# Kernel tuning notes

Measured on AMD Instinct MI355X. Metric: run time of the kernel, lower is better.

Reference implementation:

```python
import jax, jax.numpy as jnp
import numpy as np
import math

FILT_LEN = 10  # all Farras / dual filters are 10-tap
INV_SQRT2 = 1.0 / math.sqrt(2.0)

# Farras first-stage analysis filters (fs_farras), shape [tree(2), lo/hi(2), 10]
_F = 0.08838834764832
_G = 0.01122679215254
_H = 0.69587998903400
FAF_NP = np.array([
    [[0.0, -_F, _F, _H, _H, _F, -_F, _G, _G, 0.0],
     [0.0, -_G, _G, _F, _F, -_H, _H, -_F, -_F, 0.0]],
    [[_G, _G, -_F, _F, _H, _H, _F, -_F, 0.0, 0.0],
     [0.0, 0.0, -_F, -_F, _H, -_H, _F, _F, _G, -_G]]], dtype=np.float32)
# Kingsbury Q-shift dual filters (duelfilt / dualfilt1), shape [tree(2), lo/hi(2), 10]
_A = 0.03516384
_B = 0.08832942
_C = 0.23389032
_D = 0.76027237
_E = 0.58751830
_K = 0.11430184
AF_NP = np.array([
    [[_A, 0.0, -_B, _C, _D, _E, 0.0, -_K, 0.0, 0.0],
     [0.0, 0.0, -_K, 0.0, _E, -_D, _C, _B, 0.0, -_A]],
    [[0.0, 0.0, -_K, 0.0, _E, _D, _C, -_B, 0.0, _A],
     [-_A, 0.0, _B, _C, -_D, _E, 0.0, -_K, 0.0, 0.0]]], dtype=np.float32)


def _afb_axis(x, lo_f, hi_f, axis):
    """1D circular analysis filter bank along spatial `axis` (1=rows, 2=cols).
    x: (B,H,W,C). Returns (lo, hi), each halved along `axis`.
    Math: x <- cshift(x,-L); y = downsample2(fullconv(x,f)); wrap-add first L taps.
    """
    N = x.shape[axis]
    L = FILT_LEN // 2
    C = x.shape[-1]
    x = jnp.roll(x, -L, axis=axis)

    def conv(f):
        kf = f[::-1].astype(x.dtype)  # lax does correlation -> flip for convolution
        if axis == 1:
            ker = jnp.tile(kf.reshape(FILT_LEN, 1, 1, 1), (1, 1, 1, C))
            pad = [(FILT_LEN - 1, FILT_LEN - 1), (0, 0)]
            strides = (2, 1)
        else:
            ker = jnp.tile(kf.reshape(1, FILT_LEN, 1, 1), (1, 1, 1, C))
            pad = [(0, 0), (FILT_LEN - 1, FILT_LEN - 1)]
            strides = (1, 2)
        return jax.lax.conv_general_dilated(
            x, ker, window_strides=strides, padding=pad,
            dimension_numbers=('NHWC', 'HWIO', 'NHWC'),
            feature_group_count=C)  # depthwise, per-channel identical filter

    def wrap(y):
        # y has N//2 + L samples along axis; fold periodic tail into head
        head = (jax.lax.slice_in_dim(y, 0, L, axis=axis)
                + jax.lax.slice_in_dim(y, N // 2, N // 2 + L, axis=axis))
        body = jax.lax.slice_in_dim(y, L, N // 2, axis=axis)
        return jnp.concatenate([head, body], axis=axis)

    return wrap(conv(lo_f)), wrap(conv(hi_f))


def afb2d(x, lo_row, hi_row, lo_col, hi_col):
    """2D separable analysis filter bank: returns (lo, [lohi, hilo, hihi])."""
    Lr, Hr = _afb_axis(x, lo_row, hi_row, axis=1)
    lo, w0 = _afb_axis(Lr, lo_col, hi_col, axis=2)
    w1, w2 = _afb_axis(Hr, lo_col, hi_col, axis=2)
    return lo, [w0, w1, w2]


def _add_sub(a, b):
    return (a + b) * INV_SQRT2, (a - b) * INV_SQRT2


def _dtcwt(x, Faf, af, level):
    x = x / 2
    w = [[[None, None] for _ in range(2)] for _ in range(level + 1)]
    for m in range(2):
        for n in range(2):
            lo, w[0][m][n] = afb2d(x, Faf[m, 0], Faf[m, 1], Faf[n, 0], Faf[n, 1])
            for j in range(1, level):
                lo, w[j][m][n] = afb2d(lo, af[m, 0], af[m, 1], af[n, 0], af[n, 1])
            w[level][m][n] = lo
    # combine dual trees into (approx) complex pairs
    for j in range(level):
        for s in range(3):
            w[j][0][0][s], w[j][1][1][s] = _add_sub(w[j][0][0][s], w[j][1][1][s])
            w[j][0][1][s], w[j][1][0][s] = _add_sub(w[j][0][1][s], w[j][1][0][s])
    # multiscale 2x2 tiling reassembly (concat=True path)
    wc = w
    for j in range(level - 1, 0, -1):
        for a in range(2):
            for b in range(2):
                wc[j][a][b] = jnp.concatenate([
                    jnp.concatenate([wc[j + 1][a][b], wc[j][a][b][0]], axis=2),
                    jnp.concatenate([wc[j][a][b][1], wc[j][a][b][2]], axis=2)], axis=1)
    tiles = []
    for a in range(2):
        for b in range(2):
            tiles.append(jnp.concatenate([
                jnp.concatenate([wc[1][a][b], wc[0][a][b][0]], axis=2),
                jnp.concatenate([wc[0][a][b][1], wc[0][a][b][2]], axis=2)], axis=1))
    w0, w1, w2, w3 = tiles
    return jnp.concatenate([jnp.concatenate([w0, w1], axis=2),
                            jnp.concatenate([w2, w3], axis=2)], axis=1)


def setup_inputs() -> dict:
    key = jax.random.key(0)
    x = jax.random.normal(key, (8, 512, 512, 3), dtype=jnp.float32)
    return {"x": x, "Faf": jnp.asarray(FAF_NP), "af": jnp.asarray(AF_NP), "level": 3}


def reference(x, Faf, af, level):
    return _dtcwt(x, Faf, af, int(level))
```

## Files before the change

kernel.cpp:

```cpp
#include <hip/hip_runtime.h>


#define FF 0.08838834764832f
#define GG 0.01122679215254f
#define HHc 0.69587998903400f
#define AAc 0.03516384f
#define BBc 0.08832942f
#define CCc 0.23389032f
#define DDc 0.76027237f
#define EEc 0.58751830f
#define KKc 0.11430184f

__device__ __constant__ float c_filt[2][2][2][10] = {
  {
    { {0.f,-FF, FF, HHc, HHc, FF,-FF, GG, GG, 0.f},
      {0.f,-GG, GG, FF, FF,-HHc, HHc,-FF,-FF, 0.f} },
    { {GG, GG,-FF, FF, HHc, HHc, FF,-FF, 0.f, 0.f},
      {0.f, 0.f,-FF,-FF, HHc,-HHc, FF, FF, GG,-GG} }
  },
  {
    { {AAc, 0.f,-BBc, CCc, DDc, EEc, 0.f,-KKc, 0.f, 0.f},
      {0.f, 0.f,-KKc, 0.f, EEc,-DDc, CCc, BBc, 0.f,-AAc} },
    { {0.f, 0.f,-KKc, 0.f, EEc, DDc, CCc,-BBc, 0.f, AAc},
      {-AAc, 0.f, BBc, CCc,-DDc, EEc, 0.f,-KKc, 0.f, 0.f} }
  }
};

__device__ __forceinline__ void cmb(float& a, float& b) {
  const float k = 0.70710678118654752440f;
  const float s = (a + b) * k, d = (a - b) * k;
  a = s; b = d;
}

template<int LVL, int N, int Ho, int Wo>
__global__ __launch_bounds__(256) void fused_level(
    const float* __restrict__ src,
    float* __restrict__ llout,
    float* __restrict__ out)
{
  constexpr int half = N / 2;
  constexpr int W2 = 2 * Wo + 8;
  constexpr int NF = (LVL == 0) ? 4 : 8;
  constexpr size_t ZS = (size_t)8 * N * N * 3;
  constexpr size_t ZOUT = (size_t)8 * half * half * 3;
  __shared__ float inter[Ho][W2][3][NF];

  const int jt = blockIdx.x, it = blockIdx.y, b = blockIdx.z;
  const int i0 = it * Ho, j0 = jt * Wo;
  const int tid = threadIdx.x;

  constexpr int itemsA = Ho * W2 * 3;
  for (int item = tid; item < itemsA; item += 256) {
    const int il = item / (W2 * 3);
    const int rm = item - il * (W2 * 3);
    const int wl = rm / 3;
    const int c  = rm - wl * 3;
    const int colg = (2 * j0 - 4 + wl) & (N - 1);
    const int ig = i0 + il;
    if (LVL == 0) {
      const float* sp = src + (((size_t)b * N) * N + colg) * 3 + c;
      float a0 = 0.f, a1 = 0.f, a2 = 0.f, a3 = 0.f;
#pragma unroll
      for (int t = 0; t < 10; ++t) {
        const int row = (2 * ig + 5 - t) & (N - 1);
        const float v = sp[(size_t)row * (N * 3)];
        a0 += c_filt[0][0][0][t] * v;
        a1 += c_filt[0][0][1][t] * v;
        a2 += c_filt[0][1][0][t] * v;
        a3 += c_filt[0][1][1][t] * v;
      }
      inter[il][wl][c][0] = a0 * 0.5f;
      inter[il][wl][c][1] = a1 * 0.5f;
      inter[il][wl][c][2] = a2 * 0.5f;
      inter[il][wl][c][3] = a3 * 0.5f;
    } else {
      float acc[8];
#pragma unroll
      for (int f = 0; f < 8; ++f) acc[f] = 0.f;
#pragma unroll
      for (int z = 0; z < 4; ++z) {
        const int m = z >> 1;
        const float* sp = src + (size_t)z * ZS + (((size_t)b * N) * N + colg) * 3 + c;
#pragma unroll
        for (int t = 0; t < 10; ++t) {
          const int row = (2 * ig + 5 - t) & (N - 1);
          const float v = sp[(size_t)row * (N * 3)];
          acc[2 * z]     += c_filt[1][m][0][t] * v;
          acc[2 * z + 1] += c_filt[1][m][1][t] * v;
        }
      }
#pragma unroll
      for (int f = 0; f < 8; ++f) inter[il][wl][c][f] = acc[f];
    }
  }
  __syncthreads();

  constexpr int itemsB = Ho * Wo * 3;
  for (int item = tid; item < itemsB; item += 256) {
    const int il = item / (Wo * 3);
    const int rm = item - il * (Wo * 3);
    const int jl = rm / 3;
    const int c  = rm - jl * 3;
    float LL[4] = {}, LH[4] = {}, HL[4] = {}, HH[4] = {};
#pragma unroll
    for (int s = 0; s < 10; ++s) {
      const int wl = 2 * jl + 9 - s;
      if (LVL == 0) {
        const float lo0 = inter[il][wl][c][0], hi0 = inter[il][wl][c][1];
        const float lo1 = inter[il][wl][c][2], hi1 = inter[il][wl][c][3];
#pragma unroll
        for (int n = 0; n < 2; ++n) {
          const float fl = c_filt[0][n][0][s], fh = c_filt[0][n][1][s];
          LL[n]     += fl * lo0; LH[n]     += fh * lo0;
          HL[n]     += fl * hi0; HH[n]     += fh * hi0;
          LL[2 + n] += fl * lo1; LH[2 + n] += fh * lo1;
          HL[2 + n] += fl * hi1; HH[2 + n] += fh * hi1;
        }
      } else {
#pragma unroll
        for (int z = 0; z < 4; ++z) {
          const int n = z & 1;
          const float fl = c_filt[1][n][0][s], fh = c_filt[1][n][1][s];
          const float a = inter[il][wl][c][2 * z], d = inter[il][wl][c][2 * z + 1];
          LL[z] += fl * a; LH[z] += fh * a;
          HL[z] += fl * d; HH[z] += fh * d;
        }
      }
    }
    cmb(LH[0], LH[3]); cmb(LH[1], LH[2]);
    cmb(HL[0], HL[3]); cmb(HL[1], HL[2]);
    cmb(HH[0], HH[3]); cmb(HH[1], HH[2]);
    const int ig = i0 + il, jg = j0 + jl;
    const size_t outB = (size_t)b * (1024u * 1024u * 3u);
#pragma unroll
    for (int z = 0; z < 4; ++z) {
      const int m = z >> 1, n = z & 1;
      const int r0 = m * 512, c0 = n * 512;
      if (LVL == 2)
        out[outB + ((size_t)(r0 + ig) * 1024 + (c0 + jg)) * 3 + c] = LL[z];
      else
        llout[(size_t)z * ZOUT + (((size_t)b * half + ig) * half + jg) * 3 + c] = LL[z];
      out[outB + ((size_t)(r0 + ig) * 1024 + (c0 + half + jg)) * 3 + c] = LH[z];
      out[outB + ((size_t)(r0 + half + ig) * 1024 + (c0 + jg)) * 3 + c] = HL[z];
      out[outB + ((size_t)(r0 + half + ig) * 1024 + (c0 + half + jg)) * 3 + c] = HH[z];
    }
  }
}

extern "C" void kernel_launch(void* const* d_in, const int* in_sizes, int n_in,
                              void* d_out, int out_size, void* d_ws, size_t ws_size,
                              hipStream_t stream) {
  (void)in_sizes; (void)n_in; (void)out_size; (void)ws_size;
  const float* x = (const float*)d_in[0];
  float* out = (float*)d_out;
  float* LL1 = (float*)d_ws;
  float* LL2 = LL1 + 6291456;

  fused_level<0, 512, 8, 32><<<dim3(8, 32, 8), 256, 0, stream>>>(x, LL1, out);
  fused_level<1, 256, 8, 16><<<dim3(8, 16, 8), 256, 0, stream>>>(LL1, LL2, out);
  fused_level<2, 128, 8, 16><<<dim3(4, 8, 8), 256, 0, stream>>>(LL2, nullptr, out);
}
```

Measured before the change: 167.5 us.

## Vectorize row-filter loads with float4 and swizzle shared intermediate layout

The row-filter stage now treats each image row as a flat channel-interleaved float array. Each thread loads four consecutive floats with one float4 access instead of one scalar per (column, channel). The intermediate subbands are stored in shared memory as XOR-swizzled float4 entries, which reduces bank conflicts and allows vector reads. The column stage now gives each thread all three channels of one output pixel. This cuts index arithmetic and shared loads, but leaves half the threads idle at levels 1 and 2 and raises register pressure.

After: 166.2 us. No clear change (-0.8%).

```diff
diff --git a/kernel.cpp b/kernel.cpp
--- a/kernel.cpp
+++ b/kernel.cpp
@@ -32,6 +32,8 @@
   a = s; b = d;
 }
 
+__device__ __forceinline__ int swz4(int f4) { return f4 ^ ((f4 >> 3) & 7); }
+
 template<int LVL, int N, int Ho, int Wo>
 __global__ __launch_bounds__(256) void fused_level(
     const float* __restrict__ src,
@@ -41,108 +43,143 @@
   constexpr int half = N / 2;
   constexpr int W2 = 2 * Wo + 8;
   constexpr int NF = (LVL == 0) ? 4 : 8;
+  constexpr int ROWF = 3 * N;
+  constexpr int FL = 3 * W2;
+  constexpr int SIF4 = (3 * W2 * NF) / 4 + 4;
   constexpr size_t ZS = (size_t)8 * N * N * 3;
   constexpr size_t ZOUT = (size_t)8 * half * half * 3;
-  __shared__ float inter[Ho][W2][3][NF];
+  __shared__ __align__(16) float inter[Ho * SIF4 * 4];
 
   const int jt = blockIdx.x, it = blockIdx.y, b = blockIdx.z;
   const int i0 = it * Ho, j0 = jt * Wo;
   const int tid = threadIdx.x;
 
-  constexpr int itemsA = Ho * W2 * 3;
-  for (int item = tid; item < itemsA; item += 256) {
-    const int il = item / (W2 * 3);
-    const int rm = item - il * (W2 * 3);
-    const int wl = rm / 3;
-    const int c  = rm - wl * 3;
-    const int colg = (2 * j0 - 4 + wl) & (N - 1);
+  int base = (2 * j0 - 4) * 3;
+  if (base < 0) base += ROWF;
+
+  constexpr int I4 = FL / 4;
+  for (int item = tid; item < Ho * I4; item += 256) {
+    const int il = item / I4;
+    const int q4 = (item - il * I4) * 4;
+    int fg = base + q4;
+    if (fg >= ROWF) fg -= ROWF;
     const int ig = i0 + il;
-    if (LVL == 0) {
-      const float* sp = src + (((size_t)b * N) * N + colg) * 3 + c;
-      float a0 = 0.f, a1 = 0.f, a2 = 0.f, a3 = 0.f;
+    float acc[NF][4];
+#pragma unroll
+    for (int f = 0; f < NF; ++f)
+#pragma unroll
+      for (int k = 0; k < 4; ++k) acc[f][k] = 0.f;
+
+    if constexpr (LVL == 0) {
+      const float* sp = src + (size_t)b * N * ROWF + fg;
 #pragma unroll
       for (int t = 0; t < 10; ++t) {
-        const int row = (2 * ig + 5 - t) & (N - 1);
-        const float v = sp[(size_t)row * (N * 3)];
-        a0 += c_filt[0][0][0][t] * v;
-        a1 += c_filt[0][0][1][t] * v;
-        a2 += c_filt[0][1][0][t] * v;
-        a3 += c_filt[0][1][1][t] * v;
+        const int r = (2 * ig + 5 - t) & (N - 1);
+        const float4 v = *(const float4*)(sp + (size_t)r * ROWF);
+#pragma unroll
+        for (int f = 0; f < 4; ++f) {
+          const float fc = c_filt[0][f >> 1][f & 1][t];
+          acc[f][0] += fc * v.x; acc[f][1] += fc * v.y;
+          acc[f][2] += fc * v.z; acc[f][3] += fc * v.w;
+        }
       }
-      inter[il][wl][c][0] = a0 * 0.5f;
-      inter[il][wl][c][1] = a1 * 0.5f;
-      inter[il][wl][c][2] = a2 * 0.5f;
-      inter[il][wl][c][3] = a3 * 0.5f;
+#pragma unroll
+      for (int f = 0; f < 4; ++f)
+#pragma unroll
+        for (int k = 0; k < 4; ++k) acc[f][k] *= 0.5f;
     } else {
-      float acc[8];
-#pragma unroll
-      for (int f = 0; f < 8; ++f) acc[f] = 0.f;
 #pragma unroll
       for (int z = 0; z < 4; ++z) {
         const int m = z >> 1;
-        const float* sp = src + (size_t)z * ZS + (((size_t)b * N) * N + colg) * 3 + c;
+        const float* sp = src + (size_t)z * ZS + (size_t)b * N * ROWF + fg;
 #pragma unroll
         for (int t = 0; t < 10; ++t) {
-          const int row = (2 * ig + 5 - t) & (N - 1);
-          const float v = sp[(size_t)row * (N * 3)];
-          acc[2 * z]     += c_filt[1][m][0][t] * v;
-          acc[2 * z + 1] += c_filt[1][m][1][t] * v;
+          const int r = (2 * ig + 5 - t) & (N - 1);
+          const float4 v = *(const float4*)(sp + (size_t)r * ROWF);
+          const float fl = c_filt[1][m][0][t], fh = c_filt[1][m][1][t];
+          acc[2 * z][0] += fl * v.x; acc[2 * z][1] += fl * v.y;
+          acc[2 * z][2] += fl * v.z; acc[2 * z][3] += fl * v.w;
+          acc[2 * z + 1][0] += fh * v.x; acc[2 * z + 1][1] += fh * v.y;
+          acc[2 * z + 1][2] += fh * v.z; acc[2 * z + 1][3] += fh * v.w;
         }
       }
+    }
 #pragma unroll
-      for (int f = 0; f < 8; ++f) inter[il][wl][c][f] = acc[f];
+    for (int k = 0; k < 4; ++k) {
+      const int fq = q4 + k;
+      if constexpr (NF == 4) {
+        float4 w = make_float4(acc[0][k], acc[1][k], acc[2][k], acc[3][k]);
+        *(float4*)&inter[(il * SIF4 + swz4(fq)) * 4] = w;
+      } else {
+        float4 w0 = make_float4(acc[0][k], acc[1][k], acc[2][k], acc[3][k]);
+        float4 w1 = make_float4(acc[4][k], acc[5][k], acc[6][k], acc[7][k]);
+        *(float4*)&inter[(il * SIF4 + swz4(2 * fq)) * 4] = w0;
+        *(float4*)&inter[(il * SIF4 + swz4(2 * fq + 1)) * 4] = w1;
+      }
     }
   }
   __syncthreads();
 
-  constexpr int itemsB = Ho * Wo * 3;
-  for (int item = tid; item < itemsB; item += 256) {
-    const int il = item / (Wo * 3);
-    const int rm = item - il * (Wo * 3);
-    const int jl = rm / 3;
-    const int c  = rm - jl * 3;
-    float LL[4] = {}, LH[4] = {}, HL[4] = {}, HH[4] = {};
+  if (tid < Ho * Wo) {
+    const int il = tid / Wo, jl = tid - (tid / Wo) * Wo;
+    float LL[4][3] = {}, LH[4][3] = {}, HL[4][3] = {}, HH[4][3] = {};
 #pragma unroll
     for (int s = 0; s < 10; ++s) {
       const int wl = 2 * jl + 9 - s;
-      if (LVL == 0) {
-        const float lo0 = inter[il][wl][c][0], hi0 = inter[il][wl][c][1];
-        const float lo1 = inter[il][wl][c][2], hi1 = inter[il][wl][c][3];
 #pragma unroll
-        for (int n = 0; n < 2; ++n) {
-          const float fl = c_filt[0][n][0][s], fh = c_filt[0][n][1][s];
-          LL[n]     += fl * lo0; LH[n]     += fh * lo0;
-          HL[n]     += fl * hi0; HH[n]     += fh * hi0;
-          LL[2 + n] += fl * lo1; LH[2 + n] += fh * lo1;
-          HL[2 + n] += fl * hi1; HH[2 + n] += fh * hi1;
-        }
-      } else {
+      for (int c = 0; c < 3; ++c) {
+        if constexpr (LVL == 0) {
+          const int f4 = wl * 3 + c;
+          const float4 v = *(const float4*)&inter[(il * SIF4 + swz4(f4)) * 4];
+          const float a0 = v.x, d0 = v.y, a1 = v.z, d1 = v.w;
 #pragma unroll
-        for (int z = 0; z < 4; ++z) {
-          const int n = z & 1;
-          const float fl = c_filt[1][n][0][s], fh = c_filt[1][n][1][s];
-          const float a = inter[il][wl][c][2 * z], d = inter[il][wl][c][2 * z + 1];
-          LL[z] += fl * a; LH[z] += fh * a;
-          HL[z] += fl * d; HH[z] += fh * d;
+          for (int n = 0; n < 2; ++n) {
+            const float fl = c_filt[0][n][0][s], fh = c_filt[0][n][1][s];
+            LL[n][c] += fl * a0; LH[n][c] += fh * a0;
+            HL[n][c] += fl * d0; HH[n][c] += fh * d0;
+            LL[2 + n][c] += fl * a1; LH[2 + n][c] += fh * a1;
+            HL[2 + n][c] += fl * d1; HH[2 + n][c] += fh * d1;
+          }
+        } else {
+          const int f4 = (wl * 3 + c) * 2;
+          const float4 v0 = *(const float4*)&inter[(il * SIF4 + swz4(f4)) * 4];
+          const float4 v1 = *(const float4*)&inter[(il * SIF4 + swz4(f4 + 1)) * 4];
+          const float az[4] = {v0.x, v0.z, v1.x, v1.z};
+          const float dz[4] = {v0.y, v0.w, v1.y, v1.w};
+#pragma unroll
+          for (int z = 0; z < 4; ++z) {
+            const int n = z & 1;
+            const float fl = c_filt[1][n][0][s], fh = c_filt[1][n][1][s];
+            LL[z][c] += fl * az[z]; LH[z][c] += fh * az[z];
+            HL[z][c] += fl * dz[z]; HH[z][c] += fh * dz[z];
+          }
         }
       }
     }
-    cmb(LH[0], LH[3]); cmb(LH[1], LH[2]);
-    cmb(HL[0], HL[3]); cmb(HL[1], HL[2]);
-    cmb(HH[0], HH[3]); cmb(HH[1], HH[2]);
+#pragma unroll
+    for (int c = 0; c < 3; ++c) {
+      cmb(LH[0][c], LH[3][c]); cmb(LH[1][c], LH[2][c]);
+      cmb(HL[0][c], HL[3][c]); cmb(HL[1][c], HL[2][c]);
+      cmb(HH[0][c], HH[3][c]); cmb(HH[1][c], HH[2][c]);
+    }
     const int ig = i0 + il, jg = j0 + jl;
     const size_t outB = (size_t)b * (1024u * 1024u * 3u);
 #pragma unroll
     for (int z = 0; z < 4; ++z) {
       const int m = z >> 1, n = z & 1;
       const int r0 = m * 512, c0 = n * 512;
-      if (LVL == 2)
-        out[outB + ((size_t)(r0 + ig) * 1024 + (c0 + jg)) * 3 + c] = LL[z];
+      float* pLL;
+      if constexpr (LVL == 2)
+        pLL = out + outB + ((size_t)(r0 + ig) * 1024 + (c0 + jg)) * 3;
       else
-        llout[(size_t)z * ZOUT + (((size_t)b * half + ig) * half + jg) * 3 + c] = LL[z];
-      out[outB + ((size_t)(r0 + ig) * 1024 + (c0 + half + jg)) * 3 + c] = LH[z];
-      out[outB + ((size_t)(r0 + half + ig) * 1024 + (c0 + jg)) * 3 + c] = HL[z];
-      out[outB + ((size_t)(r0 + half + ig) * 1024 + (c0 + half + jg)) * 3 + c] = HH[z];
+        pLL = llout + (size_t)z * ZOUT + (((size_t)b * half + ig) * half + jg) * 3;
+      pLL[0] = LL[z][0]; pLL[1] = LL[z][1]; pLL[2] = LL[z][2];
+      float* pLH = out + outB + ((size_t)(r0 + ig) * 1024 + (c0 + half + jg)) * 3;
+      pLH[0] = LH[z][0]; pLH[1] = LH[z][1]; pLH[2] = LH[z][2];
+      float* pHL = out + outB + ((size_t)(r0 + half + ig) * 1024 + (c0 + jg)) * 3;
+      pHL[0] = HL[z][0]; pHL[1] = HL[z][1]; pHL[2] = HL[z][2];
+      float* pHH = out + outB + ((size_t)(r0 + half + ig) * 1024 + (c0 + half + jg)) * 3;
+      pHH[0] = HH[z][0]; pHH[1] = HH[z][1]; pHH[2] = HH[z][2];
     }
   }
 }
```
